# Optimization experiments

Measured on AMD Instinct MI355X. Metric: run time of the kernel, lower is better.

Reference implementation:

```python
import jax, jax.numpy as jnp
import numpy as np

EMBED = 1024
HEADS = 16
HEAD_DIM = EMBED // HEADS
CAUSAL = True
NUM_SEQS = 8
SEQ = 1024
TOTAL = NUM_SEQS * SEQ


def setup_inputs() -> dict:
    key = jax.random.key(0)
    ks = jax.random.split(key, 8)
    s = 0.02
    return {
        "hidden_states": jax.random.normal(ks[0], (TOTAL, EMBED), dtype=jnp.float32),
        "seq_len": jnp.full((NUM_SEQS,), SEQ, dtype=jnp.int64),
        "Wq": jax.random.normal(ks[1], (EMBED, EMBED), dtype=jnp.float32) * s,
        "bq": jnp.zeros((EMBED,), dtype=jnp.float32),
        "Wk": jax.random.normal(ks[2], (EMBED, EMBED), dtype=jnp.float32) * s,
        "Wv": jax.random.normal(ks[3], (EMBED, EMBED), dtype=jnp.float32) * s,
        "bv": jnp.zeros((EMBED,), dtype=jnp.float32),
        "Wo": jax.random.normal(ks[4], (EMBED, EMBED), dtype=jnp.float32) * s,
        "bo": jnp.zeros((EMBED,), dtype=jnp.float32),
    }


def _varlen_attention(q, k, v, seq_len):
    # q,k,v: [T, H, D] packed ragged tokens; seq_len: static per-sequence lengths.
    # Equivalent to the per-sequence Python loop, but done as one padded batch.
    sl = np.asarray(seq_len)
    B = sl.shape[0]
    S = int(sl.max())
    cu = np.concatenate([[0], np.cumsum(sl)])  # cu_seqlens
    pos = np.arange(S)
    # gather indices [B, S] (clipped inside each segment; invalid masked below)
    idx = cu[:-1, None] + np.minimum(pos[None, :], sl[:, None] - 1)
    valid = pos[None, :] < sl[:, None]  # [B, S]
    qp, kp, vp = q[idx], k[idx], v[idx]  # [B, S, H, D]
    scale = 1.0 / np.float32(np.sqrt(q.shape[-1]))
    scores = jnp.einsum('bqhd,bkhd->bhqk', qp, kp) * scale  # [B, H, S, S]
    mask = valid[:, None, None, :]  # valid keys
    if CAUSAL:
        mask = mask & (pos[None, :] <= pos[:, None])[None, None, :, :]
    scores = jnp.where(mask, scores, -jnp.inf)
    probs = jax.nn.softmax(scores, axis=-1)
    out = jnp.einsum('bhqk,bkhd->bqhd', probs, vp)  # [B, S, H, D]
    # unpad back to packed layout [T, H*D]
    b_of = np.repeat(np.arange(B), sl)
    p_of = np.concatenate([np.arange(l) for l in sl])
    return out[b_of, p_of].reshape(q.shape[0], -1)


def reference(hidden_states, seq_len, Wq, bq, Wk, Wv, bv, Wo, bo):
    T = hidden_states.shape[0]
    q = (hidden_states @ Wq.T + bq).reshape(T, HEADS, HEAD_DIM)
    k = (hidden_states @ Wk.T).reshape(T, HEADS, HEAD_DIM)  # k_proj has no bias
    v = (hidden_states @ Wv.T + bv).reshape(T, HEADS, HEAD_DIM)
    attn = _varlen_attention(q, k, v, seq_len)  # [T, EMBED]
    return attn @ Wo.T + bo
```

## Files before the change

### kernel.cpp

```cpp
#include <hip/hip_runtime.h>
#include <hip/hip_bf16.h>


typedef unsigned short u16;
typedef unsigned int   u32;
typedef __attribute__((ext_vector_type(8))) short bf16x8;
typedef __attribute__((ext_vector_type(4))) float f32x4;
typedef __attribute__((ext_vector_type(16))) float f32x16;
typedef __attribute__((ext_vector_type(4))) u32 u32x4;
typedef __attribute__((ext_vector_type(2))) u32 u32x2;

#define AS1 __attribute__((address_space(1)))
#define AS3 __attribute__((address_space(3)))
#define FENCE asm volatile("" ::: "memory")
#define BAR() do { FENCE; __builtin_amdgcn_s_barrier(); FENCE; } while (0)

__device__ __forceinline__ u16 f2bf(float f) {
  u32 x = __float_as_uint(f);
  x += 0x7fffu + ((x >> 16) & 1u);
  return (u16)(x >> 16);
}
__device__ __forceinline__ u32 pk2(float a, float b) {
  return (u32)f2bf(a) | ((u32)f2bf(b) << 16);
}

__global__ __launch_bounds__(256) void cvt_all(const float* __restrict__ hs,
                                               const float* __restrict__ Wq,
                                               const float* __restrict__ Wk,
                                               const float* __restrict__ Wv,
                                               const float* __restrict__ Wo,
                                               const float* __restrict__ bq,
                                               const float* __restrict__ bv,
                                               u16* __restrict__ Xb,
                                               u16* __restrict__ Wqkv,
                                               u16* __restrict__ Wob,
                                               float* __restrict__ bias) {
  if (blockIdx.x == gridDim.x - 1) {
    for (int i = threadIdx.x; i < 3072; i += 256) {
      float v = 0.f;
      if (i < 1024) v = bq[i];
      else if (i >= 2048) v = bv[i - 2048];
      bias[i] = v;
    }
  }
  int i = blockIdx.x * 256 + threadIdx.x;
  const int stride = gridDim.x * 256;
  for (; i < 3145728; i += stride) {
    const float* src;
    u16* dst;
    int off;
    if (i < 2097152) {
      src = hs; dst = Xb; off = i;
    } else {
      int j = i - 2097152;
      int m = j >> 18;
      off = j & 262143;
      src = (m == 0) ? Wq : (m == 1) ? Wk : (m == 2) ? Wv : Wo;
      dst = (m < 3) ? (Wqkv + (size_t)m * 1048576) : Wob;
    }
    float4 v = ((const float4*)src)[off];
    u32 lo = (u32)f2bf(v.x) | ((u32)f2bf(v.y) << 16);
    u32 hi = (u32)f2bf(v.z) | ((u32)f2bf(v.w) << 16);
    ((u32*)dst)[off * 2]     = lo;
    ((u32*)dst)[off * 2 + 1] = hi;
  }
}

template <int OUT_MODE>
__global__ __launch_bounds__(512, 2) void gemm8p(const u16* __restrict__ A,
                                                 const u16* __restrict__ Bw,
                                                 const float* __restrict__ bias,
                                                 void* __restrict__ C,
                                                 int M, int N, int K, int nbn) {
  __shared__ __align__(16) unsigned char smem[131072];
  auto bufA = [&](int p) -> u16* { return (u16*)(smem + (size_t)p * 16384); };
  auto bufB = [&](int p) -> u16* { return (u16*)(smem + 32768 + (size_t)p * 32768); };

  const int cpx = gridDim.x >> 3;
  const int swz = ((int)blockIdx.x & 7) * cpx + ((int)blockIdx.x >> 3);
  const int bn = swz % nbn, bm = swz / nbn;
  const int tid = threadIdx.x;
  const int l = tid & 63, w = tid >> 6;
  const int l15 = l & 15, lg = (l >> 4) & 3;
  const int wr = w >> 2, wc = w & 3;

  const u16* Ab = A + (size_t)(bm * 128) * K;
  const u16* Bb = Bw + (size_t)(bn * 256) * K;

  const int sr = w * 8 + (l >> 3);
  const int sch = (l & 7) ^ ((l >> 3) & 7);
  const int sldso = w * 64 * 8;

  auto STG = [&](const u16* src, u16* lds) {
#pragma unroll
    for (int j = 0; j < 2; ++j)
      __builtin_amdgcn_global_load_lds(
          (const AS1 void*)(src + (size_t)(j * 64 + sr) * K + sch * 8),
          (AS3 void*)((AS3 u16*)lds + j * 4096 + sldso), 16, 0, 0);
  };
  auto LDA = [&](const u16* Ah, int m, int kk) -> bf16x8 {
    int row = wr * 64 + m * 16 + l15;
    int ch = (kk * 4 + lg) ^ (l15 & 7);
    return *(const bf16x8*)&Ah[row * 64 + ch * 8];
  };
  auto LDB = [&](const u16* Bh, int n, int kk) -> bf16x8 {
    int row = wc * 64 + n * 16 + l15;
    int ch = (kk * 4 + lg) ^ (l15 & 7);
    return *(const bf16x8*)&Bh[row * 64 + ch * 8];
  };

  f32x4 acc[4][4] = {};
  const int NT = K >> 6;

  STG(Ab, bufA(0));
  STG(Bb, bufB(0));
  STG(Bb + (size_t)128 * K, bufB(0) + 8192);
  STG(Bb + 64, bufB(1));
  STG(Bb + (size_t)128 * K + 64, bufB(1) + 8192);
  asm volatile("s_waitcnt vmcnt(4)" ::: "memory");
  BAR();

  int pa = 0, pb = 0;
  for (int kt = 0; kt < NT; ++kt) {
    const u16* Ah = bufA(pa);
    const u16* Bh = bufB(pb);
    const int pa1 = pa ^ 1;
    int pb2 = pb + 2; if (pb2 >= 3) pb2 -= 3;
    bf16x8 af[4][2], bf0[2][2], bf1[2][2];

#pragma unroll
    for (int m = 0; m < 4; ++m)
#pragma unroll
      for (int kk = 0; kk < 2; ++kk) af[m][kk] = LDA(Ah, m, kk);
#pragma unroll
    for (int n = 0; n < 2; ++n)
#pragma unroll
      for (int kk = 0; kk < 2; ++kk) bf0[n][kk] = LDB(Bh, n, kk);
    if (kt + 1 < NT) STG(Ab + (kt + 1) * 64, bufA(pa1));
    if (kt + 2 < NT) STG(Bb + (kt + 2) * 64, bufB(pb2));
    BAR();
    __builtin_amdgcn_s_setprio(1);
#pragma unroll
    for (int m = 0; m < 4; ++m)
#pragma unroll
      for (int n = 0; n < 2; ++n)
#pragma unroll
        for (int kk = 0; kk < 2; ++kk)
          acc[m][n] = __builtin_amdgcn_mfma_f32_16x16x32_bf16(
              af[m][kk], bf0[n][kk], acc[m][n], 0, 0, 0);
    __builtin_amdgcn_s_setprio(0);
    BAR();

#pragma unroll
    for (int n = 0; n < 2; ++n)
#pragma unroll
      for (int kk = 0; kk < 2; ++kk) bf1[n][kk] = LDB(Bh, n + 2, kk);
    if (kt + 2 < NT) STG(Bb + (size_t)128 * K + (kt + 2) * 64, bufB(pb2) + 8192);
    BAR();
    __builtin_amdgcn_s_setprio(1);
#pragma unroll
    for (int m = 0; m < 4; ++m)
#pragma unroll
      for (int n = 0; n < 2; ++n)
#pragma unroll
        for (int kk = 0; kk < 2; ++kk)
          acc[m][n + 2] = __builtin_amdgcn_mfma_f32_16x16x32_bf16(
              af[m][kk], bf1[n][kk], acc[m][n + 2], 0, 0, 0);
    __builtin_amdgcn_s_setprio(0);
    if (kt < NT - 2) asm volatile("s_waitcnt vmcnt(4)" ::: "memory");
    else             asm volatile("s_waitcnt vmcnt(0)" ::: "memory");
    BAR();
    pa = pa1;
    pb = (pb + 1 == 3) ? 0 : pb + 1;
  }

  float* eb = (float*)smem;
  const int mychunk = wc >> 1;
#pragma unroll
  for (int ch = 0; ch < 2; ++ch) {
    __syncthreads();
    if (mychunk == ch) {
#pragma unroll
      for (int m = 0; m < 4; ++m)
#pragma unroll
        for (int n = 0; n < 4; ++n)
#pragma unroll
          for (int i = 0; i < 4; ++i)
            eb[(wr * 64 + m * 16 + lg * 4 + i) * 132 + (wc & 1) * 64 + n * 16 + l15] =
                acc[m][n][i];
    }
    __syncthreads();
#pragma unroll
    for (int ps = 0; ps < 8; ++ps) {
      int idx = (ps * 512 + tid) * 4;
      int row = idx >> 7, col = idx & 127;
      f32x4 v = *(const f32x4*)&eb[row * 132 + col];
      int colg = bn * 256 + ch * 128 + col;
      f32x4 b = *(const f32x4*)&bias[colg];
      size_t go = (size_t)(bm * 128 + row) * N + colg;
      if (OUT_MODE == 0) {
        u32x2 o;
        o[0] = pk2(v[0] + b[0], v[1] + b[1]);
        o[1] = pk2(v[2] + b[2], v[3] + b[3]);
        *(u32x2*)((u16*)C + go) = o;
      } else {
        f32x4 o = {v[0] + b[0], v[1] + b[1], v[2] + b[2], v[3] + b[3]};
        *(f32x4*)((float*)C + go) = o;
      }
    }
  }
}

__global__ __launch_bounds__(256, 4) void attn_kernel(const u16* __restrict__ qkv,
                                                      u16* __restrict__ attnout) {
  const int bid = (blockIdx.x & 7) * 128 + (blockIdx.x >> 3);
  const int qb = 7 - (bid & 7);
  const int h = (bid >> 3) & 15;
  const int s = bid >> 7;
  const int tid = threadIdx.x;
  const int l = tid & 63, w = tid >> 6;
  const int l31 = l & 31;
  const int hi = l >> 5;
  const int pb = (l >> 3) & 1;

  __shared__ __align__(16) u16 Ks[128 * 64];
  __shared__ __align__(16) u32 Vt2[64 * 65];

  const u16* kbase = qkv + (size_t)(s * 1024) * 3072 + 1024 + h * 64;
  const u16* vbase = qkv + (size_t)(s * 1024) * 3072 + 2048 + h * 64;

  bf16x8 qf[4];
  {
    const u16* qptr = qkv + (size_t)(s * 1024 + qb * 128 + w * 32 + l31) * 3072 + h * 64 + hi * 8;
#pragma unroll
    for (int c = 0; c < 4; ++c) qf[c] = *(const bf16x8*)(qptr + c * 16);
  }

  float m_r = -1e30f, l_r = 0.f;
  f32x16 o0 = {}, o1 = {};

  const int nt = qb + 1;

  const int vkv = w * 8 + (l >> 3);
  const int vd0 = (l & 7) * 8;
  const int vkp = w * 4 + (l >> 4);
  const int dEff = vd0 + pb * 4;

  const int srow = w * 8 + (l >> 3);
  const int schunk = (l & 7) ^ ((l >> 3) & 7);

  bf16x8 vcur[4], vnx[4];
#pragma unroll
  for (int p = 0; p < 4; ++p)
    vcur[p] = *(const bf16x8*)(vbase + (size_t)(p * 32 + vkv) * 3072 + vd0);

  for (int t = 0; t < nt; ++t) {
    const u16* kt = kbase + (size_t)(t * 128) * 3072;
#pragma unroll
    for (int p = 0; p < 4; ++p)
      __builtin_amdgcn_global_load_lds(
          (const AS1 void*)(kt + (size_t)(p * 32 + srow) * 3072 + schunk * 8),
          (AS3 void*)((AS3 u16*)Ks + p * 2048 + w * 512), 16, 0, 0);

#pragma unroll
    for (int p = 0; p < 4; ++p) {
      u32 dw0 = ((u32*)&vcur[p])[0], dw1 = ((u32*)&vcur[p])[1];
      u32 dw2 = ((u32*)&vcur[p])[2], dw3 = ((u32*)&vcur[p])[3];
      u32 s0 = (u32)__shfl_xor((int)(pb ? dw0 : dw2), 8, 64);
      u32 s1 = (u32)__shfl_xor((int)(pb ? dw1 : dw3), 8, 64);
      u32 md0 = pb ? dw2 : dw0, md1 = pb ? dw3 : dw1;
      u32 lo0 = pb ? s0 : md0, hi0 = pb ? md0 : s0;
      u32 lo1 = pb ? s1 : md1, hi1 = pb ? md1 : s1;
      int kp = p * 16 + vkp;
      Vt2[(dEff + 0) * 65 + kp] = (lo0 & 0xffffu) | (hi0 << 16);
      Vt2[(dEff + 1) * 65 + kp] = (lo0 >> 16) | (hi0 & 0xffff0000u);
      Vt2[(dEff + 2) * 65 + kp] = (lo1 & 0xffffu) | (hi1 << 16);
      Vt2[(dEff + 3) * 65 + kp] = (lo1 >> 16) | (hi1 & 0xffff0000u);
    }
    __syncthreads();

    if (t + 1 < nt) {
      const u16* vt = vbase + (size_t)((t + 1) * 128) * 3072;
#pragma unroll
      for (int p = 0; p < 4; ++p)
        vnx[p] = *(const bf16x8*)(vt + (size_t)(p * 32 + vkv) * 3072 + vd0);
    }

    const bool diag = (t == nt - 1);
#pragma unroll
    for (int sub = 0; sub < 4; ++sub) {
      if (!(diag && sub > w)) {
        f32x16 sc = {};
#pragma unroll
        for (int c = 0; c < 4; ++c) {
          int r = sub * 32 + l31;
          int pc = (2 * c + hi) ^ (l31 & 7);
          bf16x8 kf = *(const bf16x8*)&Ks[r * 64 + pc * 8];
          sc = __builtin_amdgcn_mfma_f32_32x32x16_bf16(kf, qf[c], sc, 0, 0, 0);
        }
        float tv[16];
#pragma unroll
        for (int r = 0; r < 16; ++r) tv[r] = sc[r] * 0.125f;
        if (diag && sub == w) {
#pragma unroll
          for (int r = 0; r < 16; ++r) {
            int kvloc = (r & 3) + 8 * (r >> 2) + 4 * hi;
            if (kvloc > l31) tv[r] = -1e30f;
          }
        }
        float t0 = fmaxf(fmaxf(tv[0], tv[1]), fmaxf(tv[2], tv[3]));
        float t1 = fmaxf(fmaxf(tv[4], tv[5]), fmaxf(tv[6], tv[7]));
        float t2 = fmaxf(fmaxf(tv[8], tv[9]), fmaxf(tv[10], tv[11]));
        float t3 = fmaxf(fmaxf(tv[12], tv[13]), fmaxf(tv[14], tv[15]));
        float tmax = fmaxf(fmaxf(t0, t1), fmaxf(t2, t3));
        tmax = fmaxf(tmax, __shfl_xor(tmax, 32, 64));
        if (!__all(tmax <= m_r + 8.0f)) {
          float nm = fmaxf(m_r, tmax);
          float alpha = __expf(m_r - nm);
          m_r = nm;
          l_r *= alpha;
#pragma unroll
          for (int r = 0; r < 16; ++r) { o0[r] *= alpha; o1[r] *= alpha; }
        }
#pragma unroll
        for (int r = 0; r < 16; ++r) tv[r] = __expf(tv[r] - m_r);
        float s0_ = (tv[0] + tv[1]) + (tv[2] + tv[3]);
        float s1_ = (tv[4] + tv[5]) + (tv[6] + tv[7]);
        float s2_ = (tv[8] + tv[9]) + (tv[10] + tv[11]);
        float s3_ = (tv[12] + tv[13]) + (tv[14] + tv[15]);
        float psum = (s0_ + s1_) + (s2_ + s3_);
        psum += __shfl_xor(psum, 32, 64);
        l_r += psum;
#pragma unroll
        for (int s01 = 0; s01 < 2; ++s01) {
          u32 W0 = pk2(tv[8 * s01 + 0], tv[8 * s01 + 1]);
          u32 W1 = pk2(tv[8 * s01 + 2], tv[8 * s01 + 3]);
          u32 X0 = pk2(tv[8 * s01 + 4], tv[8 * s01 + 5]);
          u32 X1 = pk2(tv[8 * s01 + 6], tv[8 * s01 + 7]);
          u32 rW0 = (u32)__shfl_xor((int)W0, 32, 64);
          u32 rW1 = (u32)__shfl_xor((int)W1, 32, 64);
          u32 rX0 = (u32)__shfl_xor((int)X0, 32, 64);
          u32 rX1 = (u32)__shfl_xor((int)X1, 32, 64);
          u32x4 av;
          av[0] = hi ? rX0 : W0;
          av[1] = hi ? rX1 : W1;
          av[2] = hi ? X0 : rW0;
          av[3] = hi ? X1 : rW1;
          bf16x8 pa = *(bf16x8*)&av;
          int kpb = sub * 16 + s01 * 8 + hi * 4;
          u32x4 v0 = *(const u32x4*)&Vt2[(size_t)l31 * 65 + kpb];
          o0 = __builtin_amdgcn_mfma_f32_32x32x16_bf16(pa, *(bf16x8*)&v0, o0, 0, 0, 0);
          u32x4 v1 = *(const u32x4*)&Vt2[(size_t)(32 + l31) * 65 + kpb];
          o1 = __builtin_amdgcn_mfma_f32_32x32x16_bf16(pa, *(bf16x8*)&v1, o1, 0, 0, 0);
        }
      }
    }
    __syncthreads();
#pragma unroll
    for (int p = 0; p < 4; ++p) vcur[p] = vnx[p];
  }

#pragma unroll
  for (int r = 0; r < 16; ++r) {
    int qp = (r & 3) + 8 * (r >> 2) + 4 * hi;
    float ls = __shfl(l_r, qp, 64);
    float inv = __builtin_amdgcn_rcpf(ls);
    int trow = s * 1024 + qb * 128 + w * 32 + qp;
    attnout[(size_t)trow * 1024 + h * 64 + l31]      = f2bf(o0[r] * inv);
    attnout[(size_t)trow * 1024 + h * 64 + 32 + l31] = f2bf(o1[r] * inv);
  }
}

extern "C" void kernel_launch(void* const* d_in, const int* in_sizes, int n_in,
                              void* d_out, int out_size, void* d_ws, size_t ws_size,
                              hipStream_t stream) {
  const float* hs = (const float*)d_in[0];
  const float* Wq = (const float*)d_in[2];
  const float* bq = (const float*)d_in[3];
  const float* Wk = (const float*)d_in[4];
  const float* Wv = (const float*)d_in[5];
  const float* bv = (const float*)d_in[6];
  const float* Wo = (const float*)d_in[7];
  const float* bo = (const float*)d_in[8];

  char* ws = (char*)d_ws;
  u16* Xb    = (u16*)ws;
  u16* Wqkv  = (u16*)(ws + 16777216);
  u16* Wob   = (u16*)(ws + 23068672);
  float* bqk = (float*)(ws + 25165824);
  u16* qkv   = (u16*)(ws + 25178112);
  u16* attn  = (u16*)(ws + 75509760);

  cvt_all<<<2048, 256, 0, stream>>>(hs, Wq, Wk, Wv, Wo, bq, bv, Xb, Wqkv, Wob, bqk);

  gemm8p<0><<<768, 512, 0, stream>>>(Xb, Wqkv, bqk, qkv, 8192, 3072, 1024, 12);

  attn_kernel<<<1024, 256, 0, stream>>>(qkv, attn);

  gemm8p<1><<<256, 512, 0, stream>>>(attn, Wob, bo, d_out, 8192, 1024, 1024, 4);
}
```

Measured before the change: 252.4 us.

## Make GEMM persistent with simpler double-buffered K loop and smaller LDS

Rewrites the GEMM as a persistent kernel in which each of 256 blocks loops over NTILES output tiles (3 for the QKV projection, 1 for the output projection), so the QKV launch drops from 768 to 256 blocks. The K loop changes from a split-B three-stage pipeline to a plain two-stage double buffer: all A and B fragments are loaded at once, the loop waits for every outstanding global load, then prefetches the tile two steps ahead. Shared memory is cut from 128KB to 96KB. The simpler pipeline with a full vmcnt(0) wait each iteration may expose more global-load latency, and persistence removes the tail of the 768-block launch at the cost of serialising tiles within each block.

```diff
diff --git a/kernel.cpp b/kernel.cpp
--- a/kernel.cpp
+++ b/kernel.cpp
@@ -66,26 +66,21 @@
   }
 }
 
-template <int OUT_MODE>
-__global__ __launch_bounds__(512, 2) void gemm8p(const u16* __restrict__ A,
-                                                 const u16* __restrict__ Bw,
-                                                 const float* __restrict__ bias,
-                                                 void* __restrict__ C,
-                                                 int M, int N, int K, int nbn) {
-  __shared__ __align__(16) unsigned char smem[131072];
+template <int OUT_MODE, int NTILES>
+__global__ __launch_bounds__(512, 2) void gemmP(const u16* __restrict__ A,
+                                                const u16* __restrict__ Bw,
+                                                const float* __restrict__ bias,
+                                                void* __restrict__ C,
+                                                int M, int N, int K, int nbn) {
+  __shared__ __align__(16) unsigned char smem[98304];
   auto bufA = [&](int p) -> u16* { return (u16*)(smem + (size_t)p * 16384); };
   auto bufB = [&](int p) -> u16* { return (u16*)(smem + 32768 + (size_t)p * 32768); };
 
-  const int cpx = gridDim.x >> 3;
-  const int swz = ((int)blockIdx.x & 7) * cpx + ((int)blockIdx.x >> 3);
-  const int bn = swz % nbn, bm = swz / nbn;
+  const int swz = ((int)blockIdx.x & 7) * 32 + ((int)blockIdx.x >> 3);
   const int tid = threadIdx.x;
   const int l = tid & 63, w = tid >> 6;
   const int l15 = l & 15, lg = (l >> 4) & 3;
   const int wr = w >> 2, wc = w & 3;
-
-  const u16* Ab = A + (size_t)(bm * 128) * K;
-  const u16* Bb = Bw + (size_t)(bn * 256) * K;
 
   const int sr = w * 8 + (l >> 3);
   const int sch = (l & 7) ^ ((l >> 3) & 7);
@@ -109,105 +104,97 @@
     return *(const bf16x8*)&Bh[row * 64 + ch * 8];
   };
 
-  f32x4 acc[4][4] = {};
   const int NT = K >> 6;
 
-  STG(Ab, bufA(0));
-  STG(Bb, bufB(0));
-  STG(Bb + (size_t)128 * K, bufB(0) + 8192);
-  STG(Bb + 64, bufB(1));
-  STG(Bb + (size_t)128 * K + 64, bufB(1) + 8192);
-  asm volatile("s_waitcnt vmcnt(4)" ::: "memory");
-  BAR();
-
-  int pa = 0, pb = 0;
-  for (int kt = 0; kt < NT; ++kt) {
-    const u16* Ah = bufA(pa);
-    const u16* Bh = bufB(pb);
-    const int pa1 = pa ^ 1;
-    int pb2 = pb + 2; if (pb2 >= 3) pb2 -= 3;
-    bf16x8 af[4][2], bf0[2][2], bf1[2][2];
-
-#pragma unroll
-    for (int m = 0; m < 4; ++m)
-#pragma unroll
-      for (int kk = 0; kk < 2; ++kk) af[m][kk] = LDA(Ah, m, kk);
-#pragma unroll
-    for (int n = 0; n < 2; ++n)
-#pragma unroll
-      for (int kk = 0; kk < 2; ++kk) bf0[n][kk] = LDB(Bh, n, kk);
-    if (kt + 1 < NT) STG(Ab + (kt + 1) * 64, bufA(pa1));
-    if (kt + 2 < NT) STG(Bb + (kt + 2) * 64, bufB(pb2));
+#pragma unroll 1
+  for (int ti = 0; ti < NTILES; ++ti) {
+    const int t = swz + ti * 256;
+    const int bn = t % nbn, bm = t / nbn;
+    const u16* Ab = A + (size_t)(bm * 128) * K;
+    const u16* Bb = Bw + (size_t)(bn * 256) * K;
+
+    STG(Ab, bufA(0));
+    STG(Bb, bufB(0));
+    STG(Bb + (size_t)128 * K, bufB(0) + 8192);
+    STG(Ab + 64, bufA(1));
+    STG(Bb + 64, bufB(1));
+    STG(Bb + (size_t)128 * K + 64, bufB(1) + 8192);
+    asm volatile("s_waitcnt vmcnt(0)" ::: "memory");
     BAR();
-    __builtin_amdgcn_s_setprio(1);
-#pragma unroll
-    for (int m = 0; m < 4; ++m)
-#pragma unroll
-      for (int n = 0; n < 2; ++n)
-#pragma unroll
-        for (int kk = 0; kk < 2; ++kk)
-          acc[m][n] = __builtin_amdgcn_mfma_f32_16x16x32_bf16(
-              af[m][kk], bf0[n][kk], acc[m][n], 0, 0, 0);
-    __builtin_amdgcn_s_setprio(0);
-    BAR();
-
-#pragma unroll
-    for (int n = 0; n < 2; ++n)
-#pragma unroll
-      for (int kk = 0; kk < 2; ++kk) bf1[n][kk] = LDB(Bh, n + 2, kk);
-    if (kt + 2 < NT) STG(Bb + (size_t)128 * K + (kt + 2) * 64, bufB(pb2) + 8192);
-    BAR();
-    __builtin_amdgcn_s_setprio(1);
-#pragma unroll
-    for (int m = 0; m < 4; ++m)
-#pragma unroll
-      for (int n = 0; n < 2; ++n)
-#pragma unroll
-        for (int kk = 0; kk < 2; ++kk)
-          acc[m][n + 2] = __builtin_amdgcn_mfma_f32_16x16x32_bf16(
-              af[m][kk], bf1[n][kk], acc[m][n + 2], 0, 0, 0);
-    __builtin_amdgcn_s_setprio(0);
-    if (kt < NT - 2) asm volatile("s_waitcnt vmcnt(4)" ::: "memory");
-    else             asm volatile("s_waitcnt vmcnt(0)" ::: "memory");
-    BAR();
-    pa = pa1;
-    pb = (pb + 1 == 3) ? 0 : pb + 1;
-  }
-
-  float* eb = (float*)smem;
-  const int mychunk = wc >> 1;
-#pragma unroll
-  for (int ch = 0; ch < 2; ++ch) {
+
+    f32x4 acc[4][4] = {};
+
+#pragma unroll 1
+    for (int kt = 0; kt < NT; ++kt) {
+      const int p = kt & 1;
+      const u16* Ah = bufA(p);
+      const u16* Bh = bufB(p);
+      bf16x8 af[4][2], bf[4][2];
+#pragma unroll
+      for (int m = 0; m < 4; ++m)
+#pragma unroll
+        for (int kk = 0; kk < 2; ++kk) af[m][kk] = LDA(Ah, m, kk);
+#pragma unroll
+      for (int n = 0; n < 4; ++n)
+#pragma unroll
+        for (int kk = 0; kk < 2; ++kk) bf[n][kk] = LDB(Bh, n, kk);
+      asm volatile("s_waitcnt lgkmcnt(0)" ::: "memory");
+      __builtin_amdgcn_sched_barrier(0);
+      asm volatile("s_waitcnt vmcnt(0)" ::: "memory");
+      BAR();
+      if (kt + 2 < NT) {
+        STG(Ab + (kt + 2) * 64, bufA(p));
+        STG(Bb + (kt + 2) * 64, bufB(p));
+        STG(Bb + (size_t)128 * K + (kt + 2) * 64, bufB(p) + 8192);
+      }
+      __builtin_amdgcn_s_setprio(1);
+#pragma unroll
+      for (int m = 0; m < 4; ++m)
+#pragma unroll
+        for (int n = 0; n < 4; ++n)
+#pragma unroll
+          for (int kk = 0; kk < 2; ++kk)
+            acc[m][n] = __builtin_amdgcn_mfma_f32_16x16x32_bf16(
+                af[m][kk], bf[n][kk], acc[m][n], 0, 0, 0);
+      __builtin_amdgcn_s_setprio(0);
+    }
+
+    float* eb = (float*)smem;
+    const int mychunk = wc >> 1;
+#pragma unroll
+    for (int ch = 0; ch < 2; ++ch) {
+      __syncthreads();
+      if (mychunk == ch) {
+#pragma unroll
+        for (int m = 0; m < 4; ++m)
+#pragma unroll
+          for (int n = 0; n < 4; ++n)
+#pragma unroll
+            for (int i = 0; i < 4; ++i)
+              eb[(wr * 64 + m * 16 + lg * 4 + i) * 132 + (wc & 1) * 64 + n * 16 + l15] =
+                  acc[m][n][i];
+      }
+      __syncthreads();
+#pragma unroll
+      for (int ps = 0; ps < 8; ++ps) {
+        int idx = (ps * 512 + tid) * 4;
+        int row = idx >> 7, col = idx & 127;
+        f32x4 v = *(const f32x4*)&eb[row * 132 + col];
+        int colg = bn * 256 + ch * 128 + col;
+        f32x4 b = *(const f32x4*)&bias[colg];
+        size_t go = (size_t)(bm * 128 + row) * N + colg;
+        if (OUT_MODE == 0) {
+          u32x2 o;
+          o[0] = pk2(v[0] + b[0], v[1] + b[1]);
+          o[1] = pk2(v[2] + b[2], v[3] + b[3]);
+          *(u32x2*)((u16*)C + go) = o;
+        } else {
+          f32x4 o = {v[0] + b[0], v[1] + b[1], v[2] + b[2], v[3] + b[3]};
+          *(f32x4*)((float*)C + go) = o;
+        }
+      }
+    }
     __syncthreads();
-    if (mychunk == ch) {
-#pragma unroll
-      for (int m = 0; m < 4; ++m)
-#pragma unroll
-        for (int n = 0; n < 4; ++n)
-#pragma unroll
-          for (int i = 0; i < 4; ++i)
-            eb[(wr * 64 + m * 16 + lg * 4 + i) * 132 + (wc & 1) * 64 + n * 16 + l15] =
-                acc[m][n][i];
-    }
-    __syncthreads();
-#pragma unroll
-    for (int ps = 0; ps < 8; ++ps) {
-      int idx = (ps * 512 + tid) * 4;
-      int row = idx >> 7, col = idx & 127;
-      f32x4 v = *(const f32x4*)&eb[row * 132 + col];
-      int colg = bn * 256 + ch * 128 + col;
-      f32x4 b = *(const f32x4*)&bias[colg];
-      size_t go = (size_t)(bm * 128 + row) * N + colg;
-      if (OUT_MODE == 0) {
-        u32x2 o;
-        o[0] = pk2(v[0] + b[0], v[1] + b[1]);
-        o[1] = pk2(v[2] + b[2], v[3] + b[3]);
-        *(u32x2*)((u16*)C + go) = o;
-      } else {
-        f32x4 o = {v[0] + b[0], v[1] + b[1], v[2] + b[2], v[3] + b[3]};
-        *(f32x4*)((float*)C + go) = o;
-      }
-    }
   }
 }
 
@@ -393,9 +380,9 @@
 
   cvt_all<<<2048, 256, 0, stream>>>(hs, Wq, Wk, Wv, Wo, bq, bv, Xb, Wqkv, Wob, bqk);
 
-  gemm8p<0><<<768, 512, 0, stream>>>(Xb, Wqkv, bqk, qkv, 8192, 3072, 1024, 12);
+  gemmP<0, 3><<<256, 512, 0, stream>>>(Xb, Wqkv, bqk, qkv, 8192, 3072, 1024, 12);
 
   attn_kernel<<<1024, 256, 0, stream>>>(qkv, attn);
 
-  gemm8p<1><<<256, 512, 0, stream>>>(attn, Wob, bo, d_out, 8192, 1024, 1024, 4);
-}
+  gemmP<1, 1><<<256, 512, 0, stream>>>(attn, Wob, bo, d_out, 8192, 1024, 1024, 4);
+}
```

Result: no change. 254.6 us (+0.9%).
